# Kernel optimization log

Hardware: AMD Instinct MI355X
Metric: run time of the kernel (lower is better)

## Reference

```python
import jax, jax.numpy as jnp
import numpy as np

D_MODEL = 192; N_HEAD = 6; N_LEVELS = 3; N_POINTS = 4; D_HEAD = D_MODEL // N_HEAD
W_IMG = 1024.0; H_IMG = 1024.0
STRIDES = (8.0, 16.0, 32.0)
SIGMAS = (4.0, 2.0, 1.0)
N_FREQ = 8


def fourier_pe(coords):
    # coords [..., 2] -> [..., 4*N_FREQ]
    freqs = 2.0 ** jnp.arange(N_FREQ, dtype=jnp.float32)
    x = coords[..., 0:1] * freqs * (2.0 * jnp.pi)
    y = coords[..., 1:2] * freqs * (2.0 * jnp.pi)
    return jnp.concatenate([jnp.sin(x), jnp.cos(x), jnp.sin(y), jnp.cos(y)], axis=-1)


def bilinear_sample(feat, pts):
    # feat [B, H, d_h, Hl, Wl]; pts [B, K, R, H, M, 2] (x, y) in feature-pixel coords
    # zero padding outside the map (torch grid_sample padding_mode='zeros', align_corners=True)
    B, Hh, dh, Hl, Wl = feat.shape
    featf = feat.transpose(0, 1, 3, 4, 2).reshape(B, Hh, Hl * Wl, dh)
    x = pts[..., 0]; y = pts[..., 1]
    x0 = jnp.floor(x); y0 = jnp.floor(y)
    wx1 = x - x0; wy1 = y - y0
    wx0 = 1.0 - wx1; wy0 = 1.0 - wy1
    x0i = x0.astype(jnp.int32); y0i = y0.astype(jnp.int32)
    b_idx = jnp.arange(B)[:, None, None, None, None]
    h_idx = jnp.arange(Hh)[None, None, None, :, None]

    def gather(xi, yi):
        valid = (xi >= 0) & (xi < Wl) & (yi >= 0) & (yi < Hl)
        lin = jnp.clip(yi, 0, Hl - 1) * Wl + jnp.clip(xi, 0, Wl - 1)
        v = featf[b_idx, h_idx, lin]  # [B,K,R,H,M,dh]
        return v * valid[..., None].astype(feat.dtype)

    out = (gather(x0i, y0i) * (wx0 * wy0)[..., None]
           + gather(x0i + 1, y0i) * (wx1 * wy0)[..., None]
           + gather(x0i, y0i + 1) * (wx0 * wy1)[..., None]
           + gather(x0i + 1, y0i + 1) * (wx1 * wy1)[..., None])
    return out


def layernorm(x, g, b, eps=1e-5):
    mu = jnp.mean(x, axis=-1, keepdims=True)
    var = jnp.var(x, axis=-1, keepdims=True)
    return (x - mu) * jax.lax.rsqrt(var + eps) * g + b


def setup_inputs():
    key = jax.random.key(0)
    ks = jax.random.split(key, 16)
    B, K, R = 2, 256, 32
    H4 = W4 = 32
    s = 0.02
    inp = {}
    inp['h'] = jax.random.normal(ks[0], (B, K, D_MODEL), jnp.float32)
    inp['top_indices'] = jax.random.randint(ks[1], (B, K, R), 0, H4 * W4)
    inp['query_coords'] = jax.random.uniform(ks[2], (B, K, 2), jnp.float32) * jnp.array([W_IMG, H_IMG], jnp.float32)
    inp['g'] = jax.random.normal(ks[3], (B, H4 * W4, D_MODEL), jnp.float32)
    inp['L2_proj'] = jax.random.normal(ks[4], (B, D_MODEL, 128, 128), jnp.float32)
    inp['L3_proj'] = jax.random.normal(ks[5], (B, D_MODEL, 64, 64), jnp.float32)
    inp['L4_proj'] = jax.random.normal(ks[6], (B, D_MODEL, 32, 32), jnp.float32)
    inp['w_u_w'] = jax.random.normal(ks[7], (D_MODEL, 2 * D_MODEL + 32), jnp.float32) * s
    inp['w_u_b'] = jnp.zeros((D_MODEL,), jnp.float32)
    inp['ln_u_g'] = jnp.ones((D_MODEL,), jnp.float32)
    inp['ln_u_b'] = jnp.zeros((D_MODEL,), jnp.float32)
    inp['w_delta_w'] = jax.random.normal(ks[8], (N_HEAD * N_LEVELS * N_POINTS * 2, D_MODEL), jnp.float32) * s
    inp['w_delta_b'] = jax.random.normal(ks[9], (N_HEAD * N_LEVELS * N_POINTS * 2,), jnp.float32) * s
    inp['w_a_w'] = jax.random.normal(ks[10], (N_HEAD * N_LEVELS * N_POINTS, D_MODEL), jnp.float32) * s
    inp['w_a_b'] = jnp.zeros((N_HEAD * N_LEVELS * N_POINTS,), jnp.float32)
    inp['w_o_w'] = jax.random.normal(ks[11], (D_MODEL, D_MODEL), jnp.float32) * s
    inp['w_o_b'] = jnp.zeros((D_MODEL,), jnp.float32)
    inp['e_deform'] = jax.random.normal(ks[12], (1, 1, 1, D_MODEL), jnp.float32) * s
    return inp


def reference(h, top_indices, query_coords, g, L2_proj, L3_proj, L4_proj,
              w_u_w, w_u_b, ln_u_g, ln_u_b, w_delta_w, w_delta_b,
              w_a_w, w_a_b, w_o_w, w_o_b, e_deform):
    B, K, d = h.shape
    R = top_indices.shape[2]
    H, d_h, L, M = N_HEAD, D_HEAD, N_LEVELS, N_POINTS
    H4, W4 = L4_proj.shape[2], L4_proj.shape[3]

    # anchor pixel coordinates from L4 indices
    stride_4 = STRIDES[2]
    anchor_x = (top_indices % W4).astype(jnp.float32)
    anchor_y = (top_indices // W4).astype(jnp.float32)
    anchor_px = jnp.stack([anchor_x * stride_4 + stride_4 / 2,
                           anchor_y * stride_4 + stride_4 / 2], axis=-1)  # [B,K,R,2]

    # gather global tokens at anchors
    b_idx = jnp.arange(B)[:, None, None]
    g_r = g[b_idx, top_indices]  # [B,K,R,d]

    # relative position encoding
    delta_p = anchor_px - query_coords[:, :, None, :]
    delta_p_norm = delta_p / jnp.array([W_IMG, H_IMG], jnp.float32)
    phi = fourier_pe(delta_p_norm)  # [B,K,R,32]

    h_exp = jnp.broadcast_to(h[:, :, None, :], (B, K, R, d))
    u_input = jnp.concatenate([h_exp, g_r, phi], axis=-1)  # [B,K,R,2d+32]
    u_r = layernorm(jax.nn.gelu(jnp.einsum('bkrc,dc->bkrd', u_input, w_u_w) + w_u_b,
                                approximate=False), ln_u_g, ln_u_b)

    raw_offsets = (jnp.einsum('bkrd,od->bkro', u_r, w_delta_w) + w_delta_b
                   ).reshape(B, K, R, H, L, M, 2)
    logits = (jnp.einsum('bkrd,od->bkro', u_r, w_a_w) + w_a_b).reshape(B, K, R, H, L * M)
    weights = jax.nn.softmax(logits, axis=-1).reshape(B, K, R, H, L, M)

    proj_maps = [L2_proj, L3_proj, L4_proj]
    h_r = jnp.zeros((B, K, R, H, d_h), h.dtype)
    for l in range(L):
        feat = proj_maps[l]
        Hl, Wl = feat.shape[2], feat.shape[3]
        feat = feat.reshape(B, H, d_h, Hl, Wl)
        anchor_feat = anchor_px / STRIDES[l]  # [B,K,R,2]
        off = jnp.tanh(raw_offsets[:, :, :, :, l]) * SIGMAS[l]  # [B,K,R,H,M,2]
        pts = anchor_feat[:, :, :, None, None, :] + off  # [B,K,R,H,M,2]
        sampled = bilinear_sample(feat, pts)  # [B,K,R,H,M,d_h]
        h_r = h_r + jnp.einsum('bkrhmc,bkrhm->bkrhc', sampled, weights[:, :, :, :, l])

    h_r = h_r.reshape(B, K, R, d)
    deform_tokens = jnp.einsum('bkrd,od->bkro', h_r, w_o_w) + w_o_b + e_deform
    return deform_tokens
```

## Files before the change

### kernel.cpp

```cpp
#include <hip/hip_runtime.h>
#include <hip/hip_bf16.h>

typedef __hip_bfloat16 bf16;
typedef __attribute__((ext_vector_type(8))) short s8b;
typedef __attribute__((ext_vector_type(4))) float f32x4;
typedef __attribute__((ext_vector_type(2))) float v2f;

__device__ __forceinline__ float us2f(unsigned short u) {
  union { unsigned int i; float f; } v; v.i = ((unsigned int)u) << 16; return v.f;
}
__device__ __forceinline__ float ldf(const void* p, int i, bool f32m) {
  return f32m ? ((const float*)p)[i] : us2f(((const unsigned short*)p)[i]);
}
__device__ __forceinline__ bool sniff_f32(const void* ln_g_ones) {
  return ((const unsigned int*)ln_g_ones)[0] == 0x3F800000u;
}
__device__ __forceinline__ short f2bs(float x) {
  bf16 v = __float2bfloat16(x); short s; __builtin_memcpy(&s, &v, 2); return s;
}
__device__ __forceinline__ s8b cvt8(const float* p) {
  s8b r;
  #pragma unroll
  for (int j = 0; j < 8; ++j) r[j] = f2bs(p[j]);
  return r;
}
__device__ __forceinline__ v2f bf2x(unsigned int u) {
  union { unsigned int i; float f; } lo, hi;
  lo.i = u << 16; hi.i = u & 0xffff0000u;
  v2f r; r.x = lo.f; r.y = hi.f; return r;
}
__device__ __forceinline__ float tanh_fast(float x) {
  x = fminf(fmaxf(x, -15.f), 15.f);
  float e = __expf(2.f * x);
  return (e - 1.f) * __builtin_amdgcn_rcpf(e + 1.f);
}
__device__ __forceinline__ float gelu_fast(float x) {
  float z = fabsf(x) * 0.70710678118654752f;
  float t = __builtin_amdgcn_rcpf(fmaf(0.3275911f, z, 1.f));
  float poly = t * fmaf(t, fmaf(t, fmaf(t, fmaf(t, 1.061405429f, -1.453152027f),
                                        1.421413741f), -0.284496736f), 0.254829592f);
  float erfz = 1.f - poly * __expf(-z * z);
  float s = (x >= 0.f) ? erfz : -erfz;
  return 0.5f * x * (1.f + s);
}

__global__ __launch_bounds__(256) void prep_all(
    const void* __restrict__ wu,  const void* __restrict__ wub,
    const void* __restrict__ lng, const void* __restrict__ lnb,
    const void* __restrict__ wd,  const void* __restrict__ wdb,
    const void* __restrict__ wa,  const void* __restrict__ wab,
    const void* __restrict__ wo,  const void* __restrict__ wob,
    const void* __restrict__ ed,
    const void* __restrict__ L2, const void* __restrict__ L3,
    const void* __restrict__ L4,
    bf16* __restrict__ wb1, bf16* __restrict__ wb2, bf16* __restrict__ wb3,
    float* __restrict__ wu_b, float* __restrict__ ln_g, float* __restrict__ ln_b,
    float* __restrict__ wda_b, float* __restrict__ wo_be,
    bf16* __restrict__ f2, bf16* __restrict__ f3, bf16* __restrict__ f4,
    const int useT)
{
  __shared__ float tile[64][65];
  const bool f32m = sniff_f32(lng);
  const int t = threadIdx.x;
  int bid = blockIdx.x;

  if (bid < 301) {
    if (bid < 96) {
      const int r0 = bid * 2;
      #pragma unroll
      for (int e = t; e < 832; e += 256) {
        int row = r0 + (e >= 416);
        int c = e - ((e >= 416) ? 416 : 0);
        int ks = c >> 5, r32 = c & 31, q = r32 >> 3, j = r32 & 7;
        int lane = q * 16 + (row & 15), nt = row >> 4;
        wb1[((ks * 12 + nt) * 64 + lane) * 8 + j] =
            __float2bfloat16(ldf(wu, row * 416 + c, f32m));
      }
    } else if (bid < 204) {
      const int o0 = (bid - 96) * 2;
      #pragma unroll
      for (int e = t; e < 384; e += 256) {
        int o = o0 + (e >= 192);
        int c = e - ((e >= 192) ? 192 : 0);
        float v = (o < 144) ? ldf(wd, o * 192 + c, f32m)
                            : ldf(wa, (o - 144) * 192 + c, f32m);
        int ks = c >> 5, r32 = c & 31, q = r32 >> 3, j = r32 & 7;
        int lane = q * 16 + (o & 15), nt = o >> 4;
        wb2[((ks * 14 + nt) * 64 + lane) * 8 + j] = __float2bfloat16(v);
      }
    } else if (bid < 300) {
      const int r0 = (bid - 204) * 2;
      #pragma unroll
      for (int e = t; e < 384; e += 256) {
        int row = r0 + (e >= 192);
        int c = e - ((e >= 192) ? 192 : 0);
        int ks = c >> 5, r32 = c & 31, q = r32 >> 3, j = r32 & 7;
        int lane = q * 16 + (row & 15), nt = row >> 4;
        wb3[((ks * 12 + nt) * 64 + lane) * 8 + j] =
            __float2bfloat16(ldf(wo, row * 192 + c, f32m));
      }
    } else {
      if (t < 192) {
        wu_b[t]  = ldf(wub, t, f32m);
        ln_g[t]  = ldf(lng, t, f32m);
        ln_b[t]  = ldf(lnb, t, f32m);
        wo_be[t] = ldf(wob, t, f32m) + ldf(ed, t, f32m);
      }
      if (t < 216) wda_b[t] = (t < 144) ? ldf(wdb, t, f32m) : ldf(wab, t - 144, f32m);
    }
    return;
  }

  if (!useT) return;
  int fid = bid - 301;
  const void* src; bf16* dst; int HW, spt;
  if (fid < 1536)      { src = L2; dst = f2; HW = 16384; spt = 256; }
  else if (fid < 1920) { fid -= 1536; src = L3; dst = f3; HW = 4096; spt = 64; }
  else                 { fid -= 1920; src = L4; dst = f4; HW = 1024; spt = 16; }
  int ct = fid % 3; fid /= 3;
  int st = fid % spt; int b = fid / spt;
  int sp0 = st * 64, ch0 = ct * 64;
  int q = t & 3, ch = t >> 2;

  if (f32m) {
    const float* srcf = (const float*)src + (size_t)(b * 192 + ch0 + ch) * HW + sp0;
    #pragma unroll
    for (int i = 0; i < 4; ++i) {
      int p0 = q * 16 + i * 4;
      float4 v = *(const float4*)&srcf[p0];
      tile[p0 + 0][ch] = v.x;
      tile[p0 + 1][ch] = v.y;
      tile[p0 + 2][ch] = v.z;
      tile[p0 + 3][ch] = v.w;
    }
  } else {
    const unsigned short* srcu =
        (const unsigned short*)src + (size_t)(b * 192 + ch0 + ch) * HW + sp0;
    #pragma unroll
    for (int i = 0; i < 4; ++i) {
      int p0 = q * 16 + i * 4;
      #pragma unroll
      for (int k = 0; k < 4; ++k) tile[p0 + k][ch] = us2f(srcu[p0 + k]);
    }
  }
  __syncthreads();
  #pragma unroll
  for (int i = 0; i < 2; ++i) {
    int u = t + 256 * i;
    int p = u >> 3, c8 = u & 7;
    s8b pk = cvt8(&tile[p][c8 * 8]);
    *(s8b*)&dst[(size_t)(b * HW + sp0 + p) * 192 + ch0 + c8 * 8] = pk;
  }
}

__global__ __launch_bounds__(384) void fused_k(
    const int* __restrict__ topi, const void* __restrict__ qc,
    const void* __restrict__ g, const void* __restrict__ h,
    const bf16* __restrict__ wb1, const bf16* __restrict__ wb2,
    const bf16* __restrict__ wb3,
    const float* __restrict__ wu_b,
    const float* __restrict__ ln_g, const float* __restrict__ ln_b,
    const float* __restrict__ wda_b, const float* __restrict__ wo_be,
    const void* __restrict__ lng_raw,
    const bf16* __restrict__ f2, const bf16* __restrict__ f3,
    const bf16* __restrict__ f4,
    const void* __restrict__ L2, const void* __restrict__ L3,
    const void* __restrict__ L4, const int useT,
    float* __restrict__ out)
{
  __shared__ float uni[16 * 216];
  __shared__ float u_sh[16][196];
  __shared__ float anch[16][2];
  __shared__ int   idx_sh[16];
  __shared__ float qxy[2];
  __shared__ float stats[16][2];
  __shared__ short h_sh[192];
  short* gpb = (short*)uni;
  float* ol  = uni;

  const bool f32m = sniff_f32(lng_raw);
  const int t = threadIdx.x;
  const int lane = t & 63, wv = t >> 6;
  const int m16 = lane & 15, quad = lane >> 4;
  const int bk = blockIdx.x >> 1;
  const int b = bk >> 8;
  const int tok0 = blockIdx.x * 16;

  if (t < 2) qxy[t] = ldf(qc, bk * 2 + t, f32m);
  if (t < 16) {
    int idx = topi[tok0 + t];
    idx_sh[t] = idx;
    anch[t][0] = (float)(idx & 31) * 32.f + 16.f;
    anch[t][1] = (float)(idx >> 5) * 32.f + 16.f;
  }
  if (f32m && t < 192) h_sh[t] = f2bs(((const float*)h)[bk * 192 + t]);
  __syncthreads();

  if (f32m) {
    #pragma unroll
    for (int i = 0; i < 2; ++i) {
      int u = t + 384 * i;
      int r = u / 48, q4 = u - r * 48;
      const float* s4 = (const float*)g + (size_t)(b * 1024 + idx_sh[r]) * 192 + 4 * q4;
      float4 v = *(const float4*)s4;
      short pk[4] = { f2bs(v.x), f2bs(v.y), f2bs(v.z), f2bs(v.w) };
      *(uint2*)&gpb[r * 232 + 4 * q4] = *(const uint2*)pk;
    }
  } else {
    for (int u = t; u < 16 * 192; u += 384) {
      int r = u / 192, j = u - r * 192;
      gpb[r * 232 + j] = f2bs(ldf(g, (b * 1024 + idx_sh[r]) * 192 + j, f32m));
    }
  }
  for (int u = t; u < 16 * 32; u += 384) {
    int r = u >> 5, j = u & 31;
    float dn = (((j & 16) ? (anch[r][1] - qxy[1]) : (anch[r][0] - qxy[0]))) * (1.f / 1024.f);
    float rev = dn * (float)(1 << (j & 7));
    rev = rev - floorf(rev);
    float v = (j & 8) ? __builtin_amdgcn_cosf(rev) : __builtin_amdgcn_sinf(rev);
    gpb[r * 232 + 192 + j] = f2bs(v);
  }
  __syncthreads();

  {
    const s8b* wbv = (const s8b*)wb1;
    const int nt0 = wv * 2, nt1 = wv * 2 + 1;
    float b0 = wu_b[nt0 * 16 + m16], b1 = wu_b[nt1 * 16 + m16];
    f32x4 acc0 = { b0, b0, b0, b0 };
    f32x4 acc1 = { b1, b1, b1, b1 };
    s8b bcur0 = wbv[nt0 * 64 + lane];
    s8b bcur1 = wbv[nt1 * 64 + lane];
    #pragma unroll
    for (int ks = 0; ks < 13; ++ks) {
      s8b bnx0, bnx1;
      if (ks < 12) {
        bnx0 = wbv[((ks + 1) * 12 + nt0) * 64 + lane];
        bnx1 = wbv[((ks + 1) * 12 + nt1) * 64 + lane];
      }
      s8b a;
      if (ks < 6) {
        if (f32m) {
          a = *(const s8b*)&h_sh[ks * 32 + quad * 8];
        } else {
          a = *(const s8b*)((const unsigned short*)h + bk * 192 + ks * 32 + quad * 8);
        }
      } else {
        a = *(const s8b*)&gpb[m16 * 232 + (ks - 6) * 32 + quad * 8];
      }
      acc0 = __builtin_amdgcn_mfma_f32_16x16x32_bf16(a, bcur0, acc0, 0, 0, 0);
      acc1 = __builtin_amdgcn_mfma_f32_16x16x32_bf16(a, bcur1, acc1, 0, 0, 0);
      bcur0 = bnx0; bcur1 = bnx1;
    }
    #pragma unroll
    for (int reg = 0; reg < 4; ++reg) {
      u_sh[quad * 4 + reg][nt0 * 16 + m16] = gelu_fast(acc0[reg]);
      u_sh[quad * 4 + reg][nt1 * 16 + m16] = gelu_fast(acc1[reg]);
    }
  }
  __syncthreads();

  if (t < 256) {
    int r = t >> 4, i = t & 15;
    float s = 0.f, s2 = 0.f;
    #pragma unroll
    for (int j = 0; j < 12; ++j) { float v = u_sh[r][i * 12 + j]; s += v; s2 += v * v; }
    #pragma unroll
    for (int d = 8; d >= 1; d >>= 1) { s += __shfl_xor(s, d); s2 += __shfl_xor(s2, d); }
    if (i == 0) {
      float mu = s * (1.f / 192.f);
      float var = s2 * (1.f / 192.f) - mu * mu;
      stats[r][0] = mu; stats[r][1] = rsqrtf(var + 1e-5f);
    }
  }
  __syncthreads();
  for (int u = t; u < 16 * 192; u += 384) {
    int r = u / 192, dd = u - r * 192;
    u_sh[r][dd] = (u_sh[r][dd] - stats[r][0]) * stats[r][1] * ln_g[dd] + ln_b[dd];
  }
  __syncthreads();

  {
    s8b afr[6];
    #pragma unroll
    for (int ks = 0; ks < 6; ++ks)
      afr[ks] = cvt8(&u_sh[m16][ks * 32 + quad * 8]);
    const s8b* wbv = (const s8b*)wb2;
    #pragma unroll
    for (int i = 0; i < 3; ++i) {
      int ntile = wv + 6 * i;
      if (ntile < 14) {
        int o0 = ntile * 16 + m16;
        float bias = (o0 < 216) ? wda_b[o0] : 0.f;
        f32x4 acc = { bias, bias, bias, bias };
        #pragma unroll
        for (int ks = 0; ks < 6; ++ks) {
          s8b bfr = wbv[(ks * 14 + ntile) * 64 + lane];
          acc = __builtin_amdgcn_mfma_f32_16x16x32_bf16(afr[ks], bfr, acc, 0, 0, 0);
        }
        if (o0 < 216) {
          #pragma unroll
          for (int reg = 0; reg < 4; ++reg)
            ol[(quad * 4 + reg) * 216 + o0] = acc[reg];
        }
      }
    }
  }
  __syncthreads();

  for (int u = t; u < 16 * 144; u += 384) {
    int r = u / 144, o = u - r * 144;
    int l = (o >> 3) % 3;
    ol[r * 216 + o] = tanh_fast(ol[r * 216 + o]) * (float)(4 >> l);
  }
  if (t < 96) {
    int r = t / 6, hh = t - r * 6;
    float* lg = &ol[r * 216 + 144 + hh * 12];
    float mx = lg[0];
    for (int i = 1; i < 12; ++i) mx = fmaxf(mx, lg[i]);
    float s = 0.f;
    for (int i = 0; i < 12; ++i) { float e = __expf(lg[i] - mx); lg[i] = e; s += e; }
    float inv = __builtin_amdgcn_rcpf(s);
    for (int i = 0; i < 12; ++i) lg[i] *= inv;
  }
  __syncthreads();

  {
    int tl = t / 24, c8 = t - tl * 24;
    int hc0 = c8 * 8;
    int hh = hc0 >> 5;
    float ax = anch[tl][0], ay = anch[tl][1];
    const float* olp = &ol[tl * 216];
    v2f acc2[4];
    #pragma unroll
    for (int p = 0; p < 4; ++p) { acc2[p].x = 0.f; acc2[p].y = 0.f; }

    const bf16* ftsT[3] = { f2, f3, f4 };
    const void* ftsO[3] = { L2, L3, L4 };
    #pragma unroll
    for (int l = 0; l < 3; ++l) {
      const int Hl = 128 >> l;
      const bf16* ftT = ftsT[l];
      const void* ftO = ftsO[l];
      float inv_s = 1.f / (float)(8 << l);
      float bx = ax * inv_s, by = ay * inv_s;
      #pragma unroll
      for (int m = 0; m < 4; ++m) {
        int ob = ((hh * 3 + l) * 4 + m) * 2;
        float px = bx + olp[ob];
        float py = by + olp[ob + 1];
        float fx = floorf(px), fy = floorf(py);
        int x0 = (int)fx, y0 = (int)fy;
        float wx1 = px - fx, wy1 = py - fy;
        float wx0 = 1.f - wx1, wy0 = 1.f - wy1;
        int xc0 = min(max(x0, 0), Hl - 1),   xc1 = min(max(x0 + 1, 0), Hl - 1);
        int yc0 = min(max(y0, 0), Hl - 1),   yc1 = min(max(y0 + 1, 0), Hl - 1);
        bool vx0 = (x0 >= 0) & (x0 < Hl),    vx1 = (x0 + 1 >= 0) & (x0 + 1 < Hl);
        bool vy0 = (y0 >= 0) & (y0 < Hl),    vy1 = (y0 + 1 >= 0) & (y0 + 1 < Hl);
        float aw = olp[144 + hh * 12 + l * 4 + m];
        float w00 = (vx0 && vy0) ? wx0 * wy0 * aw : 0.f;
        float w01 = (vx1 && vy0) ? wx1 * wy0 * aw : 0.f;
        float w10 = (vx0 && vy1) ? wx0 * wy1 * aw : 0.f;
        float w11 = (vx1 && vy1) ? wx1 * wy1 * aw : 0.f;
        if (useT) {
          uint4 u00 = *(const uint4*)&ftT[((b * Hl + yc0) * Hl + xc0) * 192 + hc0];
          uint4 u01 = *(const uint4*)&ftT[((b * Hl + yc0) * Hl + xc1) * 192 + hc0];
          uint4 u10 = *(const uint4*)&ftT[((b * Hl + yc1) * Hl + xc0) * 192 + hc0];
          uint4 u11 = *(const uint4*)&ftT[((b * Hl + yc1) * Hl + xc1) * 192 + hc0];
          const unsigned int* a0 = (const unsigned int*)&u00;
          const unsigned int* a1 = (const unsigned int*)&u01;
          const unsigned int* a2 = (const unsigned int*)&u10;
          const unsigned int* a3 = (const unsigned int*)&u11;
          #pragma unroll
          for (int p = 0; p < 4; ++p) {
            acc2[p] += bf2x(a0[p]) * w00;
            acc2[p] += bf2x(a1[p]) * w01;
            acc2[p] += bf2x(a2[p]) * w10;
            acc2[p] += bf2x(a3[p]) * w11;
          }
        } else {
          #pragma unroll
          for (int p = 0; p < 4; ++p) {
            #pragma unroll
            for (int e = 0; e < 2; ++e) {
              int ch = hc0 + 2 * p + e;
              float s = ldf(ftO, ((b * 192 + ch) * Hl + yc0) * Hl + xc0, f32m) * w00
                      + ldf(ftO, ((b * 192 + ch) * Hl + yc0) * Hl + xc1, f32m) * w01
                      + ldf(ftO, ((b * 192 + ch) * Hl + yc1) * Hl + xc0, f32m) * w10
                      + ldf(ftO, ((b * 192 + ch) * Hl + yc1) * Hl + xc1, f32m) * w11;
              if (e == 0) acc2[p].x += s; else acc2[p].y += s;
            }
          }
        }
      }
    }
    #pragma unroll
    for (int p = 0; p < 4; ++p) {
      u_sh[tl][hc0 + 2 * p]     = acc2[p].x;
      u_sh[tl][hc0 + 2 * p + 1] = acc2[p].y;
    }
  }
  __syncthreads();

  {
    s8b afr[6];
    #pragma unroll
    for (int ks = 0; ks < 6; ++ks)
      afr[ks] = cvt8(&u_sh[m16][ks * 32 + quad * 8]);
    const s8b* wbv = (const s8b*)wb3;
    #pragma unroll
    for (int nt = 0; nt < 2; ++nt) {
      int ntile = wv * 2 + nt;
      int n = ntile * 16 + m16;
      float bias = wo_be[n];
      f32x4 acc = { bias, bias, bias, bias };
      #pragma unroll
      for (int ks = 0; ks < 6; ++ks) {
        s8b bfr = wbv[(ks * 12 + ntile) * 64 + lane];
        acc = __builtin_amdgcn_mfma_f32_16x16x32_bf16(afr[ks], bfr, acc, 0, 0, 0);
      }
      #pragma unroll
      for (int reg = 0; reg < 4; ++reg)
        out[(long long)(tok0 + quad * 4 + reg) * 192 + n] = acc[reg];
    }
  }
}

extern "C" void kernel_launch(void* const* d_in, const int* in_sizes, int n_in,
                              void* d_out, int out_size, void* d_ws, size_t ws_size,
                              hipStream_t stream)
{
  const void* h    = d_in[0];
  const int*  topi = (const int*)d_in[1];
  const void* qc   = d_in[2];
  const void* g    = d_in[3];
  const void* L2p  = d_in[4];
  const void* L3p  = d_in[5];
  const void* L4p  = d_in[6];
  const void* wu   = d_in[7];
  const void* wub  = d_in[8];
  const void* lng  = d_in[9];
  const void* lnb  = d_in[10];
  const void* wd   = d_in[11];
  const void* wdb  = d_in[12];
  const void* wa   = d_in[13];
  const void* wab  = d_in[14];
  const void* wo   = d_in[15];
  const void* wob  = d_in[16];
  const void* ed   = d_in[17];
  float* outp = (float*)d_out;

  char* ws = (char*)d_ws;
  size_t off = 0;
  auto take = [&](size_t bytes) {
    char* p = ws + off;
    off += (bytes + 255) & ~(size_t)255;
    return p;
  };
  bf16*  wb1     = (bf16*)take(13ULL * 12 * 64 * 8 * 2);
  bf16*  wb2     = (bf16*)take(6ULL * 14 * 64 * 8 * 2);
  bf16*  wb3     = (bf16*)take(6ULL * 12 * 64 * 8 * 2);
  float* wu_bf   = (float*)take(192 * 4);
  float* lngf    = (float*)take(192 * 4);
  float* lnbf    = (float*)take(192 * 4);
  float* wda_b   = (float*)take(216 * 4);
  float* wo_be   = (float*)take(192 * 4);
  size_t feat_bytes = (2ULL * 192 * 128 * 128 + 2ULL * 192 * 64 * 64 + 2ULL * 192 * 32 * 32) * 2 + 1024;
  int useT = (ws_size >= off + feat_bytes) ? 1 : 0;
  bf16* f2 = (bf16*)take(useT ? 2ULL * 192 * 128 * 128 * 2 : 0);
  bf16* f3 = (bf16*)take(useT ? 2ULL * 192 * 64 * 64 * 2 : 0);
  bf16* f4 = (bf16*)take(useT ? 2ULL * 192 * 32 * 32 * 2 : 0);
  (void)in_sizes; (void)n_in; (void)out_size;

  hipLaunchKernelGGL(prep_all, dim3(301 + 2016), dim3(256), 0, stream,
                     wu, wub, lng, lnb, wd, wdb, wa, wab, wo, wob, ed,
                     L2p, L3p, L4p,
                     wb1, wb2, wb3, wu_bf, lngf, lnbf, wda_b, wo_be,
                     f2, f3, f4, useT);
  hipLaunchKernelGGL(fused_k, dim3(1024), dim3(384), 0, stream,
                     topi, qc, g, h, wb1, wb2, wb3, wu_bf,
                     lngf, lnbf, wda_b, wo_be, lng,
                     f2, f3, f4, L2p, L3p, L4p, useT, outp);
}
```

Baseline: 161.6 us.

## Merge weight/feature prep into main kernel via cooperative grid sync

Folds the prep kernel's weight repacking and feature-map transposition into the fused kernel. The work runs before a grid-wide cooperative sync, overlapping it with the gather/PE setup and removing one kernel launch boundary. A non-cooperative two-launch path is kept as a fallback. Risks include the cost of the grid barrier, lower occupancy if 1024 blocks must be co-resident, and the added register and code pressure in the main kernel.

```diff
diff --git a/kernel.cpp b/kernel.cpp
--- a/kernel.cpp
+++ b/kernel.cpp
@@ -1,5 +1,6 @@
 #include <hip/hip_runtime.h>
 #include <hip/hip_bf16.h>
+#include <hip/hip_cooperative_groups.h>
 
 typedef __hip_bfloat16 bf16;
 typedef __attribute__((ext_vector_type(8))) short s8b;
@@ -67,36 +68,33 @@
   if (bid < 301) {
     if (bid < 96) {
       const int r0 = bid * 2;
-      #pragma unroll
       for (int e = t; e < 832; e += 256) {
         int row = r0 + (e >= 416);
         int c = e - ((e >= 416) ? 416 : 0);
         int ks = c >> 5, r32 = c & 31, q = r32 >> 3, j = r32 & 7;
-        int lane = q * 16 + (row & 15), nt = row >> 4;
-        wb1[((ks * 12 + nt) * 64 + lane) * 8 + j] =
+        int ln2 = q * 16 + (row & 15), nt = row >> 4;
+        wb1[((ks * 12 + nt) * 64 + ln2) * 8 + j] =
             __float2bfloat16(ldf(wu, row * 416 + c, f32m));
       }
     } else if (bid < 204) {
       const int o0 = (bid - 96) * 2;
-      #pragma unroll
       for (int e = t; e < 384; e += 256) {
         int o = o0 + (e >= 192);
         int c = e - ((e >= 192) ? 192 : 0);
         float v = (o < 144) ? ldf(wd, o * 192 + c, f32m)
                             : ldf(wa, (o - 144) * 192 + c, f32m);
         int ks = c >> 5, r32 = c & 31, q = r32 >> 3, j = r32 & 7;
-        int lane = q * 16 + (o & 15), nt = o >> 4;
-        wb2[((ks * 14 + nt) * 64 + lane) * 8 + j] = __float2bfloat16(v);
+        int ln2 = q * 16 + (o & 15), nt = o >> 4;
+        wb2[((ks * 14 + nt) * 64 + ln2) * 8 + j] = __float2bfloat16(v);
       }
     } else if (bid < 300) {
       const int r0 = (bid - 204) * 2;
-      #pragma unroll
       for (int e = t; e < 384; e += 256) {
         int row = r0 + (e >= 192);
         int c = e - ((e >= 192) ? 192 : 0);
         int ks = c >> 5, r32 = c & 31, q = r32 >> 3, j = r32 & 7;
-        int lane = q * 16 + (row & 15), nt = row >> 4;
-        wb3[((ks * 12 + nt) * 64 + lane) * 8 + j] =
+        int ln2 = q * 16 + (row & 15), nt = row >> 4;
+        wb3[((ks * 12 + nt) * 64 + ln2) * 8 + j] =
             __float2bfloat16(ldf(wo, row * 192 + c, f32m));
       }
     } else {
@@ -153,19 +151,22 @@
   }
 }
 
-__global__ __launch_bounds__(384) void fused_k(
+__global__ __launch_bounds__(384) void fused_all(
     const int* __restrict__ topi, const void* __restrict__ qc,
     const void* __restrict__ g, const void* __restrict__ h,
-    const bf16* __restrict__ wb1, const bf16* __restrict__ wb2,
-    const bf16* __restrict__ wb3,
-    const float* __restrict__ wu_b,
-    const float* __restrict__ ln_g, const float* __restrict__ ln_b,
-    const float* __restrict__ wda_b, const float* __restrict__ wo_be,
-    const void* __restrict__ lng_raw,
-    const bf16* __restrict__ f2, const bf16* __restrict__ f3,
-    const bf16* __restrict__ f4,
+    const void* __restrict__ wu,  const void* __restrict__ wub,
+    const void* __restrict__ lng, const void* __restrict__ lnb,
+    const void* __restrict__ wd,  const void* __restrict__ wdb,
+    const void* __restrict__ wa,  const void* __restrict__ wab,
+    const void* __restrict__ wo,  const void* __restrict__ wob,
+    const void* __restrict__ ed,
+    bf16* __restrict__ wb1, bf16* __restrict__ wb2, bf16* __restrict__ wb3,
+    float* __restrict__ wu_b, float* __restrict__ ln_gs, float* __restrict__ ln_bs,
+    float* __restrict__ wda_b, float* __restrict__ wo_be,
+    bf16* __restrict__ f2, bf16* __restrict__ f3, bf16* __restrict__ f4,
     const void* __restrict__ L2, const void* __restrict__ L3,
-    const void* __restrict__ L4, const int useT,
+    const void* __restrict__ L4,
+    const int useT, const int coop,
     float* __restrict__ out)
 {
   __shared__ float uni[16 * 216];
@@ -177,14 +178,16 @@
   __shared__ short h_sh[192];
   short* gpb = (short*)uni;
   float* ol  = uni;
-
-  const bool f32m = sniff_f32(lng_raw);
+  short* tile_bf = (short*)&u_sh[0][0];
+
+  const bool f32m = sniff_f32(lng);
   const int t = threadIdx.x;
   const int lane = t & 63, wv = t >> 6;
   const int m16 = lane & 15, quad = lane >> 4;
-  const int bk = blockIdx.x >> 1;
+  const int bid = blockIdx.x;
+  const int bk = bid >> 1;
   const int b = bk >> 8;
-  const int tok0 = blockIdx.x * 16;
+  const int tok0 = bid * 16;
 
   if (t < 2) qxy[t] = ldf(qc, bk * 2 + t, f32m);
   if (t < 16) {
@@ -220,7 +223,99 @@
     float v = (j & 8) ? __builtin_amdgcn_cosf(rev) : __builtin_amdgcn_sinf(rev);
     gpb[r * 232 + 192 + j] = f2bs(v);
   }
-  __syncthreads();
+
+  if (coop) {
+    if (bid < 96) {
+      const int r0 = bid * 2;
+      for (int e = t; e < 832; e += 384) {
+        int row = r0 + (e >= 416);
+        int c = e - ((e >= 416) ? 416 : 0);
+        int ks = c >> 5, r32 = c & 31, q = r32 >> 3, j = r32 & 7;
+        int ln2 = q * 16 + (row & 15), nt = row >> 4;
+        wb1[((ks * 12 + nt) * 64 + ln2) * 8 + j] =
+            __float2bfloat16(ldf(wu, row * 416 + c, f32m));
+      }
+    } else if (bid < 204) {
+      const int o0 = (bid - 96) * 2;
+      for (int e = t; e < 384; e += 384) {
+        int o = o0 + (e >= 192);
+        int c = e - ((e >= 192) ? 192 : 0);
+        float v = (o < 144) ? ldf(wd, o * 192 + c, f32m)
+                            : ldf(wa, (o - 144) * 192 + c, f32m);
+        int ks = c >> 5, r32 = c & 31, q = r32 >> 3, j = r32 & 7;
+        int ln2 = q * 16 + (o & 15), nt = o >> 4;
+        wb2[((ks * 14 + nt) * 64 + ln2) * 8 + j] = __float2bfloat16(v);
+      }
+    } else if (bid < 300) {
+      const int r0 = (bid - 204) * 2;
+      for (int e = t; e < 384; e += 384) {
+        int row = r0 + (e >= 192);
+        int c = e - ((e >= 192) ? 192 : 0);
+        int ks = c >> 5, r32 = c & 31, q = r32 >> 3, j = r32 & 7;
+        int ln2 = q * 16 + (row & 15), nt = row >> 4;
+        wb3[((ks * 12 + nt) * 64 + ln2) * 8 + j] =
+            __float2bfloat16(ldf(wo, row * 192 + c, f32m));
+      }
+    } else if (bid == 300) {
+      if (t < 192) {
+        wu_b[t]   = ldf(wub, t, f32m);
+        ln_gs[t]  = ldf(lng, t, f32m);
+        ln_bs[t]  = ldf(lnb, t, f32m);
+        wo_be[t]  = ldf(wob, t, f32m) + ldf(ed, t, f32m);
+      }
+      if (t < 216) wda_b[t] = (t < 144) ? ldf(wdb, t, f32m) : ldf(wab, t - 144, f32m);
+    }
+
+    if (useT) {
+      for (int tid2 = bid; tid2 < 2016; tid2 += 1024) {
+        int fid = tid2;
+        const void* src; bf16* dst; int HW, spt;
+        if (fid < 1536)      { src = L2; dst = f2; HW = 16384; spt = 256; }
+        else if (fid < 1920) { fid -= 1536; src = L3; dst = f3; HW = 4096; spt = 64; }
+        else                 { fid -= 1920; src = L4; dst = f4; HW = 1024; spt = 16; }
+        int ct = fid % 3; fid /= 3;
+        int st = fid % spt; int bb = fid / spt;
+        int sp0 = st * 64, ch0 = ct * 64;
+        __syncthreads();
+        if (t < 256) {
+          int q = t & 3, ch = t >> 2;
+          if (f32m) {
+            const float* srcf = (const float*)src + (size_t)(bb * 192 + ch0 + ch) * HW + sp0;
+            #pragma unroll
+            for (int i = 0; i < 4; ++i) {
+              int p0 = q * 16 + i * 4;
+              float4 v = *(const float4*)&srcf[p0];
+              tile_bf[(p0 + 0) * 72 + ch] = f2bs(v.x);
+              tile_bf[(p0 + 1) * 72 + ch] = f2bs(v.y);
+              tile_bf[(p0 + 2) * 72 + ch] = f2bs(v.z);
+              tile_bf[(p0 + 3) * 72 + ch] = f2bs(v.w);
+            }
+          } else {
+            const unsigned short* srcu =
+                (const unsigned short*)src + (size_t)(bb * 192 + ch0 + ch) * HW + sp0;
+            #pragma unroll
+            for (int i = 0; i < 4; ++i) {
+              int p0 = q * 16 + i * 4;
+              #pragma unroll
+              for (int k = 0; k < 4; ++k)
+                tile_bf[(p0 + k) * 72 + ch] = (short)srcu[p0 + k];
+            }
+          }
+        }
+        __syncthreads();
+        for (int u = t; u < 512; u += 384) {
+          int p = u >> 3, c8 = u & 7;
+          uint4 pk = *(const uint4*)&tile_bf[p * 72 + c8 * 8];
+          *(uint4*)&dst[(size_t)(bb * HW + sp0 + p) * 192 + ch0 + c8 * 8] = pk;
+        }
+      }
+    }
+
+    __threadfence();
+    cooperative_groups::this_grid().sync();
+  } else {
+    __syncthreads();
+  }
 
   {
     const s8b* wbv = (const s8b*)wb1;
@@ -275,7 +370,7 @@
   __syncthreads();
   for (int u = t; u < 16 * 192; u += 384) {
     int r = u / 192, dd = u - r * 192;
-    u_sh[r][dd] = (u_sh[r][dd] - stats[r][0]) * stats[r][1] * ln_g[dd] + ln_b[dd];
+    u_sh[r][dd] = (u_sh[r][dd] - stats[r][0]) * stats[r][1] * ln_gs[dd] + ln_bs[dd];
   }
   __syncthreads();
 
@@ -471,13 +566,47 @@
   bf16* f4 = (bf16*)take(useT ? 2ULL * 192 * 32 * 32 * 2 : 0);
   (void)in_sizes; (void)n_in; (void)out_size;
 
-  hipLaunchKernelGGL(prep_all, dim3(301 + 2016), dim3(256), 0, stream,
-                     wu, wub, lng, lnb, wd, wdb, wa, wab, wo, wob, ed,
-                     L2p, L3p, L4p,
-                     wb1, wb2, wb3, wu_bf, lngf, lnbf, wda_b, wo_be,
-                     f2, f3, f4, useT);
-  hipLaunchKernelGGL(fused_k, dim3(1024), dim3(384), 0, stream,
-                     topi, qc, g, h, wb1, wb2, wb3, wu_bf,
-                     lngf, lnbf, wda_b, wo_be, lng,
-                     f2, f3, f4, L2p, L3p, L4p, useT, outp);
-}
+  static int coop_ok = -1;
+  if (coop_ok < 0) {
+    int nb = 0, ncu = 0, dev = 0;
+    hipError_t e0 = hipGetDevice(&dev);
+    hipError_t e1 = hipOccupancyMaxActiveBlocksPerMultiprocessor(
+        &nb, (const void*)fused_all, 384, 0);
+    hipError_t e2 = hipDeviceGetAttribute(
+        &ncu, hipDeviceAttributeMultiprocessorCount, dev);
+    coop_ok = (e0 == hipSuccess && e1 == hipSuccess && e2 == hipSuccess &&
+               (long long)nb * ncu >= 1024) ? 1 : 0;
+  }
+
+  bool done = false;
+  if (coop_ok) {
+    int coop = 1;
+    void* args[] = {
+      (void*)&topi, (void*)&qc, (void*)&g, (void*)&h,
+      (void*)&wu, (void*)&wub, (void*)&lng, (void*)&lnb,
+      (void*)&wd, (void*)&wdb, (void*)&wa, (void*)&wab,
+      (void*)&wo, (void*)&wob, (void*)&ed,
+      (void*)&wb1, (void*)&wb2, (void*)&wb3,
+      (void*)&wu_bf, (void*)&lngf, (void*)&lnbf,
+      (void*)&wda_b, (void*)&wo_be,
+      (void*)&f2, (void*)&f3, (void*)&f4,
+      (void*)&L2p, (void*)&L3p, (void*)&L4p,
+      (void*)&useT, (void*)&coop, (void*)&outp
+    };
+    hipError_t ce = hipLaunchCooperativeKernel(
+        (const void*)fused_all, dim3(1024), dim3(384), args, 0, stream);
+    if (ce == hipSuccess) done = true; else coop_ok = 0;
+  }
+  if (!done) {
+    hipLaunchKernelGGL(prep_all, dim3(301 + 2016), dim3(256), 0, stream,
+                       wu, wub, lng, lnb, wd, wdb, wa, wab, wo, wob, ed,
+                       L2p, L3p, L4p,
+                       wb1, wb2, wb3, wu_bf, lngf, lnbf, wda_b, wo_be,
+                       f2, f3, f4, useT);
+    hipLaunchKernelGGL(fused_all, dim3(1024), dim3(384), 0, stream,
+                       topi, qc, g, h, wu, wub, lng, lnb, wd, wdb, wa, wab,
+                       wo, wob, ed, wb1, wb2, wb3, wu_bf, lngf, lnbf,
+                       wda_b, wo_be, f2, f3, f4, L2p, L3p, L4p,
+                       useT, 0, outp);
+  }
+}
```

Measured after the change: 163.7 us. No clear change (+1.2%).
